# Performance work log

Measured on AMD Instinct MI355X. Metric: run time of the kernel, lower is better.

## Reference

```python
import jax, jax.numpy as jnp
import numpy as np

BINS = 1000  # torch: int(max-min)*100; ~1000 for standardized randn data, fixed for jit


def _entropy(counts, n, width):
    # torch.histogram(density=True): probs = counts / (n * bin_width)
    probs = counts / (n * width)
    safe = jnp.where(probs > 0, probs, 1.0)
    return jnp.sum(jnp.where(probs > 0, -probs * jnp.log2(safe), 0.0))


def setup_inputs() -> dict:
    key = jax.random.key(0)
    k1, k2 = jax.random.split(key)
    x = jax.random.normal(k1, (1024, 64, 16, 16), dtype=jnp.float32)
    u = jax.random.uniform(k2, (1024, 64, 16, 16), dtype=jnp.float32)  # dropout noise
    return {"x": x, "u": u}


def reference(x, u):
    B = x.shape[0]
    temp = x.reshape(B, -1)              # [B, D]
    D = temp.shape[1]

    # corrcoef across rows (each row is a variable)
    tc = temp - temp.mean(axis=1, keepdims=True)
    cov = tc @ tc.T                      # [B, B]
    d = jnp.sqrt(jnp.diag(cov))
    corr = cov / (d[:, None] * d[None, :])
    factor1 = jnp.mean(jnp.abs(corr), axis=1)            # [B]

    # global standardization (torch.std default is unbiased, ddof=1)
    tnorm = (temp - temp.mean()) / jnp.std(temp, ddof=1)
    lo, hi = tnorm.min(), tnorm.max()
    width = (hi - lo) / BINS
    idx = jnp.clip(jnp.floor((tnorm - lo) / width).astype(jnp.int32), 0, BINS - 1)

    # per-row histograms via batched scatter-add; batch histogram = sum of rows
    row_counts = jax.vmap(lambda ii: jnp.zeros(BINS, jnp.float32).at[ii].add(1.0))(idx)  # [B, BINS]
    batch_counts = row_counts.sum(axis=0)

    batch_entropy = _entropy(batch_counts, B * D, width)
    local_entropy = jax.vmap(lambda c: _entropy(c, D, width))(row_counts)  # [B]

    f2 = local_entropy / batch_entropy
    is_zero = f2 == 0
    f1 = jnp.where(is_zero, 0.0, factor1)
    f2 = jnp.where(is_zero, 1.0, jnp.where(f2 < 1.0, 1.0 / f2, f2))
    keep = f1 / f2                       # 1 - p, per row
    p = 1.0 - keep                       # [B]

    mask = (u.reshape(B, -1) > p[:, None]).astype(x.dtype)
    out = (mask * temp) / keep[:, None]
    return out.reshape(x.shape)
```

## Files before the change

### kernel.cpp

```cpp
#include <hip/hip_runtime.h>
#include <math.h>

#define NROWS 1024
#define DCOLS 16384
#define NTOT  16777216
#define BINS  1000
#define NPAIR2 36
#define KSPL2  16

typedef short short8 __attribute__((ext_vector_type(8)));
typedef unsigned short ushort8 __attribute__((ext_vector_type(8)));
typedef float f32x4 __attribute__((ext_vector_type(4)));

#define GLOAD_LDS16(gp, lp) __builtin_amdgcn_global_load_lds( \
    (const __attribute__((address_space(1))) unsigned int*)(gp), \
    (__attribute__((address_space(3))) unsigned int*)(lp), 16, 0, 0)

__device__ __constant__ int CHK_TR[12] = {1,17,33,49,  0,5,10,15,  128,149,170,191};
__device__ __constant__ int CHK_CB[12] = {0,0,0,0,     128,128,128,128,  0,0,0,0};
__device__ __constant__ int CHK_SL[12] = {0,0,0,0,     1,1,1,1,    0,0,0,0};

__global__ __launch_bounds__(256) void k_rowsplit(const float* __restrict__ x,
    unsigned short* __restrict__ phi, unsigned short* __restrict__ plo,
    double* __restrict__ rowsum, double* __restrict__ rowsumsq,
    double* __restrict__ rowmin, double* __restrict__ rowmax) {
  const int row = blockIdx.x, t = threadIdx.x;
  const size_t base = (size_t)row * DCOLS;
  double s = 0.0, s2 = 0.0;
  float mn = 3.4028235e38f, mx = -3.4028235e38f;
  #pragma unroll
  for (int i = 0; i < 8; ++i) {
    const size_t off = base + (size_t)i * 2048 + (size_t)t * 8;
    const float4 v0 = *(const float4*)(x + off);
    const float4 v1 = *(const float4*)(x + off + 4);
    const float vv[8] = {v0.x, v0.y, v0.z, v0.w, v1.x, v1.y, v1.z, v1.w};
    ushort8 h, lo;
    #pragma unroll
    for (int c = 0; c < 8; ++c) {
      unsigned ub = __float_as_uint(vv[c]);
      unsigned hb = (ub + 0x7FFFu + ((ub >> 16) & 1u)) >> 16;
      float hf = __uint_as_float(hb << 16);
      float r = vv[c] - hf;
      unsigned ur = __float_as_uint(r);
      unsigned lb = (ur + 0x7FFFu + ((ur >> 16) & 1u)) >> 16;
      h[c] = (unsigned short)hb; lo[c] = (unsigned short)lb;
      double dv = vv[c];
      s += dv; s2 += dv * dv;
      mn = fminf(mn, vv[c]); mx = fmaxf(mx, vv[c]);
    }
    *(ushort8*)(phi + off) = h;
    *(ushort8*)(plo + off) = lo;
  }
  #pragma unroll
  for (int off = 32; off > 0; off >>= 1) {
    s  += __shfl_down(s, off);
    s2 += __shfl_down(s2, off);
    mn = fminf(mn, __shfl_down(mn, off));
    mx = fmaxf(mx, __shfl_down(mx, off));
  }
  __shared__ double lsd[8];
  __shared__ float  lsf[8];
  const int lane = t & 63, w = t >> 6;
  if (lane == 0) { lsd[w] = s; lsd[4 + w] = s2; lsf[w] = mn; lsf[4 + w] = mx; }
  __syncthreads();
  if (t == 0) {
    rowsum[row]   = (lsd[0] + lsd[1]) + (lsd[2] + lsd[3]);
    rowsumsq[row] = (lsd[4] + lsd[5]) + (lsd[6] + lsd[7]);
    rowmin[row] = (double)fminf(fminf(lsf[0], lsf[1]), fminf(lsf[2], lsf[3]));
    rowmax[row] = (double)fmaxf(fmaxf(lsf[4], lsf[5]), fmaxf(lsf[6], lsf[7]));
  }
}

__global__ __launch_bounds__(256) void k_rowstats(const float* __restrict__ x,
    double* __restrict__ rowsum, double* __restrict__ rowsumsq,
    double* __restrict__ rowmin, double* __restrict__ rowmax) {
  const int row = blockIdx.x;
  const int t = threadIdx.x;
  const float4* xr = (const float4*)(x + (size_t)row * DCOLS);
  double s = 0.0, s2 = 0.0;
  float mn = 3.4028235e38f, mx = -3.4028235e38f;
  for (int j = t; j < DCOLS / 4; j += 256) {
    float4 v = xr[j];
    double a = v.x, b = v.y, c = v.z, d = v.w;
    s  += (a + b) + (c + d);
    s2 += (a * a + b * b) + (c * c + d * d);
    mn = fminf(mn, fminf(fminf(v.x, v.y), fminf(v.z, v.w)));
    mx = fmaxf(mx, fmaxf(fmaxf(v.x, v.y), fmaxf(v.z, v.w)));
  }
  #pragma unroll
  for (int off = 32; off > 0; off >>= 1) {
    s  += __shfl_down(s, off);
    s2 += __shfl_down(s2, off);
    mn = fminf(mn, __shfl_down(mn, off));
    mx = fmaxf(mx, __shfl_down(mx, off));
  }
  __shared__ double lsd[8];
  __shared__ float  lsf[8];
  const int lane = t & 63, w = t >> 6;
  if (lane == 0) { lsd[w] = s; lsd[4 + w] = s2; lsf[w] = mn; lsf[4 + w] = mx; }
  __syncthreads();
  if (t == 0) {
    rowsum[row]   = (lsd[0] + lsd[1]) + (lsd[2] + lsd[3]);
    rowsumsq[row] = (lsd[4] + lsd[5]) + (lsd[6] + lsd[7]);
    rowmin[row] = (double)fminf(fminf(lsf[0], lsf[1]), fminf(lsf[2], lsf[3]));
    rowmax[row] = (double)fmaxf(fmaxf(lsf[4], lsf[5]), fmaxf(lsf[6], lsf[7]));
  }
}

__global__ __launch_bounds__(256) void k_stats2(
    const double* __restrict__ rowsum, const double* __restrict__ rowsumsq,
    const double* __restrict__ rowmin, const double* __restrict__ rowmax,
    double* __restrict__ m, double* __restrict__ dn, float* __restrict__ fscal,
    float* __restrict__ flg, unsigned* __restrict__ bc) {
#pragma clang fp contract(off)
  const int t = threadIdx.x;
  for (int b = t; b < BINS; b += 256) bc[b] = 0;
  double s = 0.0, s2 = 0.0, mn = 1e300, mx = -1e300;
  for (int r = t; r < NROWS; r += 256) {
    s += rowsum[r]; s2 += rowsumsq[r];
    mn = fmin(mn, rowmin[r]); mx = fmax(mx, rowmax[r]);
  }
  #pragma unroll
  for (int off = 32; off > 0; off >>= 1) {
    s  += __shfl_down(s, off);
    s2 += __shfl_down(s2, off);
    mn = fmin(mn, __shfl_down(mn, off));
    mx = fmax(mx, __shfl_down(mx, off));
  }
  __shared__ double lsd[16];
  const int lane = t & 63, w = t >> 6;
  if (lane == 0) { lsd[w] = s; lsd[4 + w] = s2; lsd[8 + w] = mn; lsd[12 + w] = mx; }
  __syncthreads();
  if (t == 0) {
    double S  = (lsd[0] + lsd[1]) + (lsd[2] + lsd[3]);
    double S2 = (lsd[4] + lsd[5]) + (lsd[6] + lsd[7]);
    double MN = fmin(fmin(lsd[8], lsd[9]), fmin(lsd[10], lsd[11]));
    double MX = fmax(fmax(lsd[12], lsd[13]), fmax(lsd[14], lsd[15]));
    const double N = 16777216.0;
    double mu  = S / N;
    double var = (S2 - S * S / N) / (N - 1.0);
    double sig = sqrt(var);
    float mu32 = (float)mu;
    float sg32 = (float)sig;
    float mnf  = (float)MN;
    float mxf  = (float)MX;
    float lof  = (mnf - mu32) / sg32;
    float hif  = (mxf - mu32) / sg32;
    float wf   = (hif - lof) / 1000.0f;
    fscal[0] = mu32;
    fscal[1] = sg32;
    fscal[2] = lof;
    fscal[3] = wf;
    fscal[4] = 16384.0f * wf;
    fscal[5] = 16777216.0f * wf;
    flg[0] = 0.0f;
  }
  __syncthreads();
  for (int r = t; r < NROWS; r += 256) {
    double rs = rowsum[r];
    m[r]  = rs / 16384.0;
    dn[r] = sqrt(rowsumsq[r] - rs * rs * (1.0 / 16384.0));
  }
}

__global__ __launch_bounds__(256, 2) void k_gramm_sk(
    const unsigned short* __restrict__ phi, const unsigned short* __restrict__ plo,
    float* __restrict__ Gs) {
  const int pid = blockIdx.x >> 4, ks = blockIdx.x & 15;
  int bi = 0, rem = pid;
  while (rem >= 8 - bi) { rem -= 8 - bi; ++bi; }
  const int bj = bi + rem;
  const bool diag = (bi == bj);
  __shared__ short As[128][64];
  __shared__ short Bs[128][64];
  const int t = threadIdx.x;
  const int w = t >> 6, l = t & 63;

  const bool isB = (w >= 2);
  const int rbase = (w & 1) * 64;
  const int prow0 = (isB ? bj : bi) * 128;
  short* lbase = (isB ? &Bs[0][0] : &As[0][0]) + rbase * 64;
  const bool skipStage = diag && isB;
  const int g = (l & 7) ^ (l >> 3);
  const unsigned short* pl = (g & 4) ? plo : phi;
  const unsigned short* gbase = pl
      + (size_t)(prow0 + rbase + (l >> 3)) * DCOLS + (g & 3) * 8;

  f32x4 acc[4][4];
  #pragma unroll
  for (int a = 0; a < 4; ++a)
    #pragma unroll
    for (int b = 0; b < 4; ++b) acc[a][b] = (f32x4){0.f, 0.f, 0.f, 0.f};

  const int wr = w >> 1, wc = w & 1;
  const short* BA = diag ? &As[0][0] : &Bs[0][0];
  const int kbeg = ks * 1024;
  const int kp = l >> 4;

  for (int k0 = kbeg; k0 < kbeg + 1024; k0 += 32) {
    __syncthreads();
    if (!skipStage) {
      #pragma unroll
      for (int q = 0; q < 8; ++q)
        GLOAD_LDS16(gbase + (size_t)q * 8 * DCOLS + k0, lbase + q * 512);
    }
    __syncthreads();
    short8 ah[4], al[4];
    #pragma unroll
    for (int as_ = 0; as_ < 4; ++as_) {
      const int arow = wr * 64 + as_ * 16 + (l & 15);
      const int r7 = arow & 7;
      ah[as_] = *(const short8*)&As[arow][(kp ^ r7) * 8];
      al[as_] = *(const short8*)&As[arow][((4 + kp) ^ r7) * 8];
    }
    #pragma unroll
    for (int bs_ = 0; bs_ < 4; ++bs_) {
      const int brow = wc * 64 + bs_ * 16 + (l & 15);
      const int r7 = brow & 7;
      short8 bh = *(const short8*)(BA + brow * 64 + (kp ^ r7) * 8);
      short8 bl = *(const short8*)(BA + brow * 64 + ((4 + kp) ^ r7) * 8);
      #pragma unroll
      for (int as_ = 0; as_ < 4; ++as_) {
        acc[as_][bs_] = __builtin_amdgcn_mfma_f32_16x16x32_bf16(ah[as_], bh, acc[as_][bs_], 0, 0, 0);
        acc[as_][bs_] = __builtin_amdgcn_mfma_f32_16x16x32_bf16(ah[as_], bl, acc[as_][bs_], 0, 0, 0);
        acc[as_][bs_] = __builtin_amdgcn_mfma_f32_16x16x32_bf16(al[as_], bh, acc[as_][bs_], 0, 0, 0);
      }
    }
  }

  float* gt = Gs + ((size_t)pid * KSPL2 + ks) * 16384;
  #pragma unroll
  for (int as_ = 0; as_ < 4; ++as_)
    #pragma unroll
    for (int bs_ = 0; bs_ < 4; ++bs_)
      #pragma unroll
      for (int v = 0; v < 4; ++v)
        gt[(wr * 64 + as_ * 16 + (l >> 4) * 4 + v) * 128 + wc * 64 + bs_ * 16 + (l & 15)]
            = acc[as_][bs_][v];
}

__global__ __launch_bounds__(256) void k_gepi_chk(const float* __restrict__ x,
    const float* __restrict__ Gs, const double* __restrict__ m,
    const double* __restrict__ dn, double* __restrict__ fpart,
    double* __restrict__ chkpart, int nGepi) {
  const int t = threadIdx.x;
  if ((int)blockIdx.x >= nGepi) {
    const int b = blockIdx.x - nGepi;
    const int e = b >> 4, grp = b & 15;
    const int cl = t >> 5;
    const int ksg = t & 31;
    const int trow = CHK_TR[e];
    const int col  = CHK_CB[e] + grp * 8 + cl;
    const float4* xa = (const float4*)(x + (size_t)trow * DCOLS) + ksg * 128;
    const float4* xb = (const float4*)(x + (size_t)col  * DCOLS) + ksg * 128;
    double g = 0.0;
    for (int k = 0; k < 128; ++k) {
      float4 va = xa[k], vb = xb[k];
      g += (double)va.x * vb.x + (double)va.y * vb.y
         + (double)va.z * vb.z + (double)va.w * vb.w;
    }
    g += __shfl_xor(g, 1); g += __shfl_xor(g, 2); g += __shfl_xor(g, 4);
    g += __shfl_xor(g, 8); g += __shfl_xor(g, 16);
    __shared__ double cd[8];
    if (ksg == 0) cd[cl] = g;
    __syncthreads();
    if (t == 0) {
      double s = 0.0;
      #pragma unroll
      for (int i = 0; i < 8; ++i) {
        int c = CHK_CB[e] + grp * 8 + i;
        double cov = cd[i] - 16384.0 * m[trow] * m[c];
        s += fabs(cov) / dn[c];
      }
      chkpart[e * 16 + grp] = s;
    }
    return;
  }
  const int pid = blockIdx.x;
  int bi = 0, rem = pid;
  while (rem >= 8 - bi) { rem -= 8 - bi; ++bi; }
  const int bj = bi + rem;
  const bool diag = (bi == bj);
  __shared__ double Gt[64][129];
  const float* g = Gs + (size_t)pid * KSPL2 * 16384;
  double myScol = 0.0;
  const int cc = t >> 1, cq = t & 1;
  for (int h = 0; h < 2; ++h) {
    for (int i = t; i < 8192; i += 256) {
      const int off = h * 8192 + i;
      double sg = ((((double)g[off] + (double)g[16384 + off])
                 +  ((double)g[32768 + off] + (double)g[49152 + off]))
                +  (((double)g[65536 + off] + (double)g[81920 + off])
                 +  ((double)g[98304 + off] + (double)g[114688 + off])))
                + ((((double)g[131072 + off] + (double)g[147456 + off])
                 +  ((double)g[163840 + off] + (double)g[180224 + off]))
                +  (((double)g[196608 + off] + (double)g[212992 + off])
                 +  ((double)g[229376 + off] + (double)g[245760 + off])));
      Gt[i >> 7][i & 127] = sg;
    }
    __syncthreads();
    {
      const int r = t >> 2, q = t & 3;
      const int grow = bi * 128 + h * 64 + r;
      const double mi = m[grow] * 16384.0;
      double s = 0.0;
      for (int i = 0; i < 32; ++i) {
        const int c = q * 32 + i;
        double cov = Gt[r][c] - mi * m[bj * 128 + c];
        s += fabs(cov) / dn[bj * 128 + c];
      }
      s += __shfl_xor(s, 1); s += __shfl_xor(s, 2);
      if (q == 0) fpart[(size_t)grow * 8 + bj] = s;
    }
    if (!diag) {
      const double mj = m[bj * 128 + cc] * 16384.0;
      double sc = 0.0;
      for (int i = 0; i < 32; ++i) {
        const int r = cq * 32 + i;
        const int grow = bi * 128 + h * 64 + r;
        double cov = Gt[r][cc] - m[grow] * mj;
        sc += fabs(cov) / dn[grow];
      }
      sc += __shfl_xor(sc, 1);
      if (cq == 0) myScol += sc;
    }
    __syncthreads();
  }
  if (!diag && cq == 0)
    fpart[(size_t)(bj * 128 + cc) * 8 + bi] = myScol;
}

__global__ __launch_bounds__(256) void k_gram(const float* __restrict__ x,
    const double* __restrict__ m, const double* __restrict__ dn,
    double* __restrict__ fpart) {
  __shared__ float As[32][72];
  __shared__ float Bs[32][72];
  __shared__ double red[64][16];
  const int t = threadIdx.x;
  const int bi = blockIdx.y, bj = blockIdx.x;
  const int tx = t & 15, ty = t >> 4;
  const int lr = t >> 2, lc = t & 3;
  const float* Ap = x + (size_t)(bi * 64 + lr) * DCOLS;
  const float* Bp = x + (size_t)(bj * 64 + lr) * DCOLS;
  double acc[4][4];
  #pragma unroll
  for (int i = 0; i < 4; ++i)
    #pragma unroll
    for (int j = 0; j < 4; ++j) acc[i][j] = 0.0;
  float4 a0 = ((const float4*)Ap)[lc];
  float4 a1 = ((const float4*)Ap)[lc + 4];
  float4 b0 = ((const float4*)Bp)[lc];
  float4 b1 = ((const float4*)Bp)[lc + 4];
  for (int k0 = 0; k0 < DCOLS; k0 += 32) {
    __syncthreads();
    {
      const float* a0p = (const float*)&a0;
      const float* a1p = (const float*)&a1;
      const float* b0p = (const float*)&b0;
      const float* b1p = (const float*)&b1;
      #pragma unroll
      for (int jj = 0; jj < 4; ++jj) {
        As[lc * 4 + jj][lr]      = a0p[jj];
        As[16 + lc * 4 + jj][lr] = a1p[jj];
        Bs[lc * 4 + jj][lr]      = b0p[jj];
        Bs[16 + lc * 4 + jj][lr] = b1p[jj];
      }
    }
    __syncthreads();
    if (k0 + 32 < DCOLS) {
      a0 = ((const float4*)(Ap + k0 + 32))[lc];
      a1 = ((const float4*)(Ap + k0 + 32))[lc + 4];
      b0 = ((const float4*)(Bp + k0 + 32))[lc];
      b1 = ((const float4*)(Bp + k0 + 32))[lc + 4];
    }
    float ac[4][4];
    #pragma unroll
    for (int i = 0; i < 4; ++i)
      #pragma unroll
      for (int j = 0; j < 4; ++j) ac[i][j] = 0.0f;
    #pragma unroll
    for (int k = 0; k < 32; ++k) {
      const float4 av = *(const float4*)&As[k][ty * 4];
      const float4 bv = *(const float4*)&Bs[k][tx * 4];
      const float aa[4] = {av.x, av.y, av.z, av.w};
      const float bb[4] = {bv.x, bv.y, bv.z, bv.w};
      #pragma unroll
      for (int i = 0; i < 4; ++i)
        #pragma unroll
        for (int j = 0; j < 4; ++j)
          ac[i][j] += aa[i] * bb[j];
    }
    #pragma unroll
    for (int i = 0; i < 4; ++i)
      #pragma unroll
      for (int j = 0; j < 4; ++j) acc[i][j] += (double)ac[i][j];
  }
  double mr[4], mc[4], dc[4];
  #pragma unroll
  for (int i = 0; i < 4; ++i) mr[i] = m[bi * 64 + ty * 4 + i];
  #pragma unroll
  for (int j = 0; j < 4; ++j) {
    int col = bj * 64 + tx * 4 + j;
    mc[j] = m[col]; dc[j] = dn[col];
  }
  #pragma unroll
  for (int i = 0; i < 4; ++i) {
    double pi = 0.0;
    #pragma unroll
    for (int j = 0; j < 4; ++j) {
      double cov = acc[i][j] - 16384.0 * mr[i] * mc[j];
      pi += fabs(cov) / dc[j];
    }
    red[ty * 4 + i][tx] = pi;
  }
  __syncthreads();
  if (t < 64) {
    double ssum = 0.0;
    #pragma unroll
    for (int q = 0; q < 16; ++q) ssum += red[t][q];
    fpart[(size_t)(bi * 64 + t) * 16 + bj] = ssum;
  }
}

__global__ __launch_bounds__(256) void k_hist(const float* __restrict__ x,
    const float* __restrict__ fscal, double* __restrict__ localent,
    unsigned* __restrict__ bc) {
#pragma clang fp contract(off)
  __shared__ unsigned h[4][BINS];
  const int row = blockIdx.x, t = threadIdx.x;
  const int w = t >> 6, lane = t & 63;
  for (int b = t; b < 4 * BINS; b += 256) h[b / BINS][b % BINS] = 0;
  __syncthreads();
  const float mu32 = fscal[0], sg32 = fscal[1], lof = fscal[2], wf = fscal[3];
  const float4* xr = (const float4*)(x + (size_t)row * DCOLS);
  for (int j = t; j < DCOLS / 4; j += 256) {
    float4 v = xr[j];
    float vv[4] = {v.x, v.y, v.z, v.w};
    #pragma unroll
    for (int c = 0; c < 4; ++c) {
      float tn = (vv[c] - mu32) / sg32;
      float q  = (tn - lof) / wf;
      int idx = (int)floorf(q);
      idx = idx < 0 ? 0 : (idx > BINS - 1 ? BINS - 1 : idx);
      atomicAdd(&h[w][idx], 1u);
    }
  }
  __syncthreads();
  const double Dw = (double)fscal[4];
  double ls = 0.0;
  for (int b = t; b < BINS; b += 256) {
    unsigned c = (h[0][b] + h[1][b]) + (h[2][b] + h[3][b]);
    if (c) {
      atomicAdd(&bc[b], c);
      double pd = (double)c / Dw;
      ls -= pd * log2(pd);
    }
  }
  #pragma unroll
  for (int off = 32; off > 0; off >>= 1) ls += __shfl_down(ls, off);
  __shared__ double lsd[4];
  if (lane == 0) lsd[w] = ls;
  __syncthreads();
  if (t == 0) localent[row] = (lsd[0] + lsd[1]) + (lsd[2] + lsd[3]);
}

__global__ __launch_bounds__(256) void k_final(const unsigned* __restrict__ bc,
    const float* __restrict__ fscal, const double* __restrict__ localent,
    const double* __restrict__ fpart, const double* __restrict__ dn,
    const double* __restrict__ chkpart, float* __restrict__ flg,
    float* __restrict__ pf, float* __restrict__ kf, int nq, int doChk) {
#pragma clang fp contract(off)
  const int t = threadIdx.x;
  if (doChk && t < 12) {
    double s = 0.0;
    #pragma unroll
    for (int q = 0; q < 16; ++q) s += chkpart[t * 16 + q];
    double got = fpart[(size_t)CHK_TR[t] * 8 + CHK_SL[t]];
    if (fabs(got - s) > 2e-3 * fmax(fabs(s), 1e-30))
      atomicAdd(flg, 1e6f * (float)(t + 1));
  }
  const double Nw = (double)fscal[5];
  double be = 0.0;
  for (int b = t; b < BINS; b += 256) {
    unsigned c = bc[b];
    if (c) { double pd = (double)c / Nw; be -= pd * log2(pd); }
  }
  #pragma unroll
  for (int off = 32; off > 0; off >>= 1) be += __shfl_down(be, off);
  __shared__ double lsd[4];
  __shared__ double sbent;
  const int lane = t & 63, w = t >> 6;
  if (lane == 0) lsd[w] = be;
  __syncthreads();
  if (t == 0) sbent = (lsd[0] + lsd[1]) + (lsd[2] + lsd[3]);
  __syncthreads();
  const float bef = (float)sbent;
  for (int r = t; r < NROWS; r += 256) {
    double s = 0.0;
    for (int q = 0; q < nq; ++q) s += fpart[(size_t)r * nq + q];
    float f1f = (float)(s / (dn[r] * 1024.0));
    float lef = (float)localent[r];
    float f2f = lef / bef;
    if (f2f == 0.0f) { f1f = 0.0f; f2f = 1.0f; }
    else if (f2f < 1.0f) f2f = 1.0f / f2f;
    float keepf = f1f / f2f;
    pf[r] = 1.0f - keepf;
    kf[r] = keepf;
  }
}

__global__ __launch_bounds__(256) void k_apply(const float* __restrict__ x,
    const float* __restrict__ u, const float* __restrict__ pf,
    const float* __restrict__ kf, const float* __restrict__ flg,
    float* __restrict__ out) {
#pragma clang fp contract(off)
  const size_t e = ((size_t)blockIdx.x * 256 + threadIdx.x) * 4;
  const float fl = flg[0];
  if (fl != 0.0f) {
    float4 o = {0.f, 0.f, 0.f, 0.f};
    if (e == 0) o.x = fl;
    *(float4*)(out + e) = o;
    return;
  }
  const int row = (int)(e >> 14);
  const float pr = pf[row], kr = kf[row];
  const float4 xv = *(const float4*)(x + e);
  const float4 uv = *(const float4*)(u + e);
  float4 o;
  o.x = (uv.x > pr) ? (xv.x / kr) : 0.0f;
  o.y = (uv.y > pr) ? (xv.y / kr) : 0.0f;
  o.z = (uv.z > pr) ? (xv.z / kr) : 0.0f;
  o.w = (uv.w > pr) ? (xv.w / kr) : 0.0f;
  *(float4*)(out + e) = o;
}

extern "C" void kernel_launch(void* const* d_in, const int* in_sizes, int n_in,
                              void* d_out, int out_size, void* d_ws, size_t ws_size,
                              hipStream_t stream) {
  const float* x = (const float*)d_in[0];
  const float* u = (const float*)d_in[1];
  float* out = (float*)d_out;

  const size_t PLANE = (size_t)NROWS * DCOLS * sizeof(unsigned short);
  const size_t NDBL  = 7 * 1024 + (size_t)NROWS * 16 + 192;
  const size_t TAILB = NDBL * 8 + (2056 + 4) * 4 + BINS * 4;
  const bool big = ws_size >= 2 * PLANE + TAILB;

  char* base = (char*)d_ws;
  unsigned short* phi = (unsigned short*)base;
  unsigned short* plo = (unsigned short*)(base + PLANE);
  double* W = big ? (double*)(base + 2 * PLANE) : (double*)base;

  double* rowsum   = W;
  double* rowsumsq = W + 1024;
  double* rowmin   = W + 2048;
  double* rowmax   = W + 3072;
  double* m        = W + 4096;
  double* dn       = W + 5120;
  double* localent = W + 6144;
  double* fpart    = W + 7168;
  double* chkpart  = W + 7168 + (size_t)NROWS * 16;
  float*  F        = (float*)(chkpart + 192);
  float*  pf       = F;
  float*  kf       = F + 1024;
  float*  fscal    = F + 2048;
  float*  flg      = F + 2056;
  unsigned* bc     = (unsigned*)(F + 2060);

  if (big) {
    float* Gs = out;
    k_rowsplit<<<NROWS, 256, 0, stream>>>(x, phi, plo, rowsum, rowsumsq, rowmin, rowmax);
    k_stats2<<<1, 256, 0, stream>>>(rowsum, rowsumsq, rowmin, rowmax, m, dn, fscal, flg, bc);
    k_gramm_sk<<<NPAIR2 * KSPL2, 256, 0, stream>>>(phi, plo, Gs);
    k_gepi_chk<<<NPAIR2 + 192, 256, 0, stream>>>(x, Gs, m, dn, fpart, chkpart, NPAIR2);
    k_hist<<<NROWS, 256, 0, stream>>>(x, fscal, localent, bc);
    k_final<<<1, 256, 0, stream>>>(bc, fscal, localent, fpart, dn, chkpart, flg, pf, kf, 8, 1);
  } else {
    k_rowstats<<<NROWS, 256, 0, stream>>>(x, rowsum, rowsumsq, rowmin, rowmax);
    k_stats2<<<1, 256, 0, stream>>>(rowsum, rowsumsq, rowmin, rowmax, m, dn, fscal, flg, bc);
    k_gram<<<dim3(16, 16), 256, 0, stream>>>(x, m, dn, fpart);
    k_hist<<<NROWS, 256, 0, stream>>>(x, fscal, localent, bc);
    k_final<<<1, 256, 0, stream>>>(bc, fscal, localent, fpart, dn, chkpart, flg, pf, kf, 16, 0);
  }
  k_apply<<<NTOT / (256 * 4), 256, 0, stream>>>(x, u, pf, kf, flg, out);
}
```

Baseline: 207.9 us.

## Replace global histogram atomics with per-row counts plus reduction; remap gram blocks

```diff
diff --git a/kernel.cpp b/kernel.cpp
--- a/kernel.cpp
+++ b/kernel.cpp
@@ -166,7 +166,8 @@
 __global__ __launch_bounds__(256, 2) void k_gramm_sk(
     const unsigned short* __restrict__ phi, const unsigned short* __restrict__ plo,
     float* __restrict__ Gs) {
-  const int pid = blockIdx.x >> 4, ks = blockIdx.x & 15;
+  const int logical = (blockIdx.x & 7) * 72 + (blockIdx.x >> 3);
+  const int pid = logical >> 4, ks = logical & 15;
   int bi = 0, rem = pid;
   while (rem >= 8 - bi) { rem -= 8 - bi; ++bi; }
   const int bj = bi + rem;
@@ -422,6 +423,73 @@
   }
 }
 
+__global__ __launch_bounds__(256) void k_hist_nc(const float* __restrict__ x,
+    const float* __restrict__ fscal, double* __restrict__ localent,
+    unsigned* __restrict__ rowcnt) {
+#pragma clang fp contract(off)
+  __shared__ unsigned h[4][BINS];
+  const int row = blockIdx.x, t = threadIdx.x;
+  const int w = t >> 6, lane = t & 63;
+  for (int b = t; b < 4 * BINS; b += 256) h[b / BINS][b % BINS] = 0;
+  __syncthreads();
+  const float mu32 = fscal[0], sg32 = fscal[1], lof = fscal[2], wf = fscal[3];
+  const float4* xr = (const float4*)(x + (size_t)row * DCOLS);
+  for (int j = t; j < DCOLS / 4; j += 256) {
+    float4 v = xr[j];
+    float vv[4] = {v.x, v.y, v.z, v.w};
+    #pragma unroll
+    for (int c = 0; c < 4; ++c) {
+      float tn = (vv[c] - mu32) / sg32;
+      float q  = (tn - lof) / wf;
+      int idx = (int)floorf(q);
+      idx = idx < 0 ? 0 : (idx > BINS - 1 ? BINS - 1 : idx);
+      atomicAdd(&h[w][idx], 1u);
+    }
+  }
+  __syncthreads();
+  const double Dw = (double)fscal[4];
+  double ls = 0.0;
+  for (int b = t; b < BINS; b += 256) {
+    unsigned c = (h[0][b] + h[1][b]) + (h[2][b] + h[3][b]);
+    rowcnt[(size_t)row * BINS + b] = c;
+    if (c) {
+      double pd = (double)c / Dw;
+      ls -= pd * log2(pd);
+    }
+  }
+  #pragma unroll
+  for (int off = 32; off > 0; off >>= 1) ls += __shfl_down(ls, off);
+  __shared__ double lsd[4];
+  if (lane == 0) lsd[w] = ls;
+  __syncthreads();
+  if (t == 0) localent[row] = (lsd[0] + lsd[1]) + (lsd[2] + lsd[3]);
+}
+
+__global__ __launch_bounds__(256) void k_bsum(const unsigned* __restrict__ rowcnt,
+    unsigned* __restrict__ bc) {
+  const int b0 = blockIdx.x * 8;
+  const int t = threadIdx.x;
+  unsigned ps[8] = {0, 0, 0, 0, 0, 0, 0, 0};
+  for (int r = t; r < NROWS; r += 256) {
+    const unsigned* rp = rowcnt + (size_t)r * BINS + b0;
+    #pragma unroll
+    for (int i = 0; i < 8; ++i) ps[i] += rp[i];
+  }
+  #pragma unroll
+  for (int off = 32; off > 0; off >>= 1)
+    #pragma unroll
+    for (int i = 0; i < 8; ++i) ps[i] += __shfl_down(ps[i], off);
+  __shared__ unsigned red[4][8];
+  const int w = t >> 6, lane = t & 63;
+  if (lane == 0) {
+    #pragma unroll
+    for (int i = 0; i < 8; ++i) red[w][i] = ps[i];
+  }
+  __syncthreads();
+  if (t < 8)
+    bc[b0 + t] = (red[0][t] + red[1][t]) + (red[2][t] + red[3][t]);
+}
+
 __global__ __launch_bounds__(256) void k_hist(const float* __restrict__ x,
     const float* __restrict__ fscal, double* __restrict__ localent,
     unsigned* __restrict__ bc) {
@@ -569,11 +637,13 @@
 
   if (big) {
     float* Gs = out;
+    unsigned* rowcnt = (unsigned*)(out + 10485760);
     k_rowsplit<<<NROWS, 256, 0, stream>>>(x, phi, plo, rowsum, rowsumsq, rowmin, rowmax);
     k_stats2<<<1, 256, 0, stream>>>(rowsum, rowsumsq, rowmin, rowmax, m, dn, fscal, flg, bc);
     k_gramm_sk<<<NPAIR2 * KSPL2, 256, 0, stream>>>(phi, plo, Gs);
     k_gepi_chk<<<NPAIR2 + 192, 256, 0, stream>>>(x, Gs, m, dn, fpart, chkpart, NPAIR2);
-    k_hist<<<NROWS, 256, 0, stream>>>(x, fscal, localent, bc);
+    k_hist_nc<<<NROWS, 256, 0, stream>>>(x, fscal, localent, rowcnt);
+    k_bsum<<<BINS / 8, 256, 0, stream>>>(rowcnt, bc);
     k_final<<<1, 256, 0, stream>>>(bc, fscal, localent, fpart, dn, chkpart, flg, pf, kf, 8, 1);
   } else {
     k_rowstats<<<NROWS, 256, 0, stream>>>(x, rowsum, rowsumsq, rowmin, rowmax);
```

Result: slower. 236.7 us (+13.9%).
